# Optimization experiments

Measured on AMD Instinct MI355X. Metric: run time of the kernel, lower is better.

## Reference

```python
import jax, jax.numpy as jnp
import numpy as np

NUM_LAYERS = 6
NUM_HEADS = 8
HIDDEN = 512
GRID_N = 32                      # num_nodes = GRID_N**2 + 1 (encoder pads a global node)
SEQ = GRID_N * GRID_N + 1        # 1025
FFN_HIDDEN = 32 * ((int(2 * HIDDEN / 3) + 31) // 32)  # 352, SwiGLU rounding
BATCH = 8
EPS = 1e-5


def build_grid_mask():
    """4-neighbor grid adjacency + self loops, padded with an all-connected first row/col."""
    n = GRID_N
    idx = np.arange(n * n).reshape(n, n)
    A = np.zeros((n * n, n * n), dtype=bool)
    # horizontal edges
    a, b = idx[:, :-1].ravel(), idx[:, 1:].ravel()
    A[a, b] = True; A[b, a] = True
    # vertical edges
    a, b = idx[:-1, :].ravel(), idx[1:, :].ravel()
    A[a, b] = True; A[b, a] = True
    np.fill_diagonal(A, True)
    M = np.ones((n * n + 1, n * n + 1), dtype=bool)
    M[1:, 1:] = A
    return jnp.asarray(M)


def setup_inputs() -> dict:
    key = jax.random.key(0)
    ks = jax.random.split(key, 9)
    std = 0.02
    D, F, L = HIDDEN, FFN_HIDDEN, NUM_LAYERS
    return {
        "x": jax.random.normal(ks[0], (BATCH, SEQ, D), dtype=jnp.float32),
        "mask": build_grid_mask(),                                  # [SEQ, SEQ] bool
        "wqkv": jax.random.normal(ks[1], (L, 3 * D, D), jnp.float32) * std,
        "wo":   jax.random.normal(ks[2], (L, D, D), jnp.float32) * std,
        "w1":   jax.random.normal(ks[3], (L, F, D), jnp.float32) * std,
        "w2":   jax.random.normal(ks[4], (L, D, F), jnp.float32) * std,
        "w3":   jax.random.normal(ks[5], (L, F, D), jnp.float32) * std,
        "attn_norm_w": jnp.ones((L, D), jnp.float32),
        "ffn_norm_w":  jnp.ones((L, D), jnp.float32),
    }


def rmsnorm(x, w):
    ms = jnp.mean(x * x, axis=-1, keepdims=True)
    return x * jax.lax.rsqrt(ms + EPS) * w


def reference(x, mask, wqkv, wo, w1, w2, w3, attn_norm_w, ffn_norm_w):
    B, S, D = x.shape
    H = NUM_HEADS
    hd = D // H
    scale = 1.0 / jnp.sqrt(jnp.asarray(hd, x.dtype))
    neg = jnp.asarray(-jnp.inf, x.dtype)
    for l in range(NUM_LAYERS):
        # --- attention ---
        h = rmsnorm(x, attn_norm_w[l])
        qkv = h @ wqkv[l].T                                   # [B,S,3D]
        q, k, v = jnp.split(qkv, 3, axis=-1)
        q = q.reshape(B, S, H, hd).transpose(0, 2, 1, 3)      # [B,H,S,hd]
        k = k.reshape(B, S, H, hd).transpose(0, 2, 1, 3)
        v = v.reshape(B, S, H, hd).transpose(0, 2, 1, 3)
        scores = jnp.einsum("bhqd,bhkd->bhqk", q, k) * scale  # [B,H,S,S]
        scores = jnp.where(mask, scores, neg)
        attn = jax.nn.softmax(scores, axis=-1)
        o = jnp.einsum("bhqk,bhkd->bhqd", attn, v)
        o = o.transpose(0, 2, 1, 3).reshape(B, S, D)
        x = x + o @ wo[l].T
        # --- SwiGLU FFN ---
        h = rmsnorm(x, ffn_norm_w[l])
        y = (jax.nn.silu(h @ w1[l].T) * (h @ w3[l].T)) @ w2[l].T
        x = x + y
    return x
```

## Files before the change

kernel.cpp:

```cpp
#include <hip/hip_runtime.h>

typedef unsigned short u16;
typedef short s8v __attribute__((ext_vector_type(8)));
typedef float f4v __attribute__((ext_vector_type(4)));

#define SEQ 1025
#define BATCH 8
#define MROWS (BATCH * SEQ)
#define D 512
#define TD 1536
#define F 352
#define F2I 768
#define FPAD 384
#define NLAYERS 6
#define QKVS ((size_t)BATCH * 8 * SEQ * 64)

__device__ __forceinline__ u16 f2b(float f) {
    unsigned u;
    __builtin_memcpy(&u, &f, 4);
    unsigned r = u + 0x7fffu + ((u >> 16) & 1u);
    return (u16)(r >> 16);
}
__device__ __forceinline__ float b2f(u16 h) {
    unsigned u = ((unsigned)h) << 16;
    float f;
    __builtin_memcpy(&f, &u, 4);
    return f;
}

__global__ __launch_bounds__(256) void convA_k(const float* __restrict__ src, u16* __restrict__ dst, int n4) {
    int i = blockIdx.x * 256 + threadIdx.x;
    if (i >= n4) return;
    float4 v = ((const float4*)src)[i];
    ushort4 r;
    r.x = f2b(v.x); r.y = f2b(v.y); r.z = f2b(v.z); r.w = f2b(v.w);
    ((ushort4*)dst)[i] = r;
}

__global__ __launch_bounds__(256) void convW13i_k(const float* __restrict__ w1, const float* __restrict__ w3, u16* __restrict__ dst) {
    int i = blockIdx.x * 256 + threadIdx.x;
    const int total = NLAYERS * F2I * (D / 4);
    if (i >= total) return;
    int k4 = i & 127;
    int rem = i >> 7;
    int n = rem % F2I, l = rem / F2I;
    int k32 = n >> 5, j = n & 31;
    int f = k32 * 16 + (j & 15);
    ushort4 r;
    if (f < F) {
        const float* src = (j < 16) ? (w1 + ((size_t)(l * F + f) * D))
                                    : (w3 + ((size_t)(l * F + f) * D));
        float4 v = ((const float4*)src)[k4];
        r.x = f2b(v.x); r.y = f2b(v.y); r.z = f2b(v.z); r.w = f2b(v.w);
    } else {
        r.x = 0; r.y = 0; r.z = 0; r.w = 0;
    }
    ((ushort4*)dst)[i] = r;
}

__global__ __launch_bounds__(256) void convW2_k(const float* __restrict__ w2, u16* __restrict__ dst) {
    int i = blockIdx.x * 256 + threadIdx.x;
    const int total = NLAYERS * D * (FPAD / 4);
    if (i >= total) return;
    int k4 = i % (FPAD / 4);
    int rem = i / (FPAD / 4);
    int n = rem % D, l = rem / D;
    ushort4 r;
    if (k4 < F / 4) {
        float4 v = ((const float4*)(w2 + (size_t)(l * D + n) * F))[k4];
        r.x = f2b(v.x); r.y = f2b(v.y); r.z = f2b(v.z); r.w = f2b(v.w);
    } else {
        r.x = 0; r.y = 0; r.z = 0; r.w = 0;
    }
    ((ushort4*)dst)[i] = r;
}

__global__ __launch_bounds__(128) void rmsnorm_k(const float* __restrict__ x, const float* __restrict__ w,
                                                 u16* __restrict__ out) {
    int row = blockIdx.x;
    int tid = threadIdx.x;
    float4 v = ((const float4*)(x + (size_t)row * D))[tid];
    float ss = v.x * v.x + v.y * v.y + v.z * v.z + v.w * v.w;
    #pragma unroll
    for (int off = 32; off; off >>= 1) ss += __shfl_xor(ss, off);
    __shared__ float red[2];
    if ((tid & 63) == 0) red[tid >> 6] = ss;
    __syncthreads();
    float rs = rsqrtf((red[0] + red[1]) * (1.0f / (float)D) + 1e-5f);
    float4 wv = ((const float4*)w)[tid];
    ushort4 pk;
    pk.x = f2b(v.x * rs * wv.x); pk.y = f2b(v.y * rs * wv.y);
    pk.z = f2b(v.z * rs * wv.z); pk.w = f2b(v.w * rs * wv.w);
    ((ushort4*)(out + (size_t)row * D))[tid] = pk;
}

#define STAGE_GEMM(bufofs, kk)                                                          \
    do {                                                                                \
        int k0_ = (kk);                                                                 \
        _Pragma("unroll")                                                               \
        for (int i_ = 0; i_ < 4; ++i_) {                                                \
            int chunk_ = i_ * 256 + tid;                                                \
            int row_ = chunk_ >> 3, kc_ = chunk_ & 7;                                   \
            int gr_ = tm + row_;                                                        \
            gr_ = gr_ < M ? gr_ : M - 1;                                                \
            const u16* srcA_ = A + (size_t)gr_ * K + k0_ + ((kc_ ^ (row_ & 7)) << 3);   \
            __builtin_amdgcn_global_load_lds(                                           \
                (const __attribute__((address_space(1))) void*)srcA_,                   \
                (__attribute__((address_space(3))) void*)(smem + (bufofs) + (size_t)(i_ * 256 + wave * 64) * 8), \
                16, 0, 0);                                                              \
            const u16* srcB_ = B + (size_t)(tn + row_) * K + k0_ + ((kc_ ^ (row_ & 7)) << 3); \
            __builtin_amdgcn_global_load_lds(                                           \
                (const __attribute__((address_space(1))) void*)srcB_,                   \
                (__attribute__((address_space(3))) void*)(smem + 16384 + (bufofs) + (size_t)(i_ * 256 + wave * 64) * 8), \
                16, 0, 0);                                                              \
        }                                                                               \
    } while (0)

template <int MODE>
__global__ __launch_bounds__(256) void gemm_bt_k(const u16* __restrict__ A, const u16* __restrict__ B,
                                                 void* __restrict__ C, int M, int K, int ldc,
                                                 int nx, int nwg) {
    __shared__ u16 smem[32768];
    const int tid = threadIdx.x;
    const int lane = tid & 63;
    const int wave = tid >> 6;
    int hw = blockIdx.x;
    int q8 = nwg >> 3, r8 = nwg & 7;
    int xcd = hw & 7, pos = hw >> 3;
    int work = (xcd < r8 ? xcd * (q8 + 1) : r8 * (q8 + 1) + (xcd - r8) * q8) + pos;
    int ty = work / nx, tx = work - ty * nx;
    const int tm = ty * 128;
    const int tn = tx * 128;
    const int wm = (wave >> 1) * 64;
    const int wn = (wave & 1) * 64;
    f4v acc[4][4] = {};

    const int nk = K >> 6;
    STAGE_GEMM(0, 0);
    __syncthreads();
    for (int k = 0; k < nk; ++k) {
        int cur = (k & 1) * 8192;
        if (k + 1 < nk) STAGE_GEMM(cur ^ 8192, (k + 1) << 6);
        const u16* sa_ = smem + cur;
        const u16* sb_ = smem + 16384 + cur;
        #pragma unroll
        for (int ks = 0; ks < 2; ++ks) {
            int kc = ks * 4 + (lane >> 4);
            s8v af[4], bfr[4];
            #pragma unroll
            for (int mi = 0; mi < 4; ++mi) {
                int row = wm + mi * 16 + (lane & 15);
                af[mi] = *(const s8v*)(sa_ + row * 64 + ((kc ^ (row & 7)) << 3));
            }
            #pragma unroll
            for (int ni = 0; ni < 4; ++ni) {
                int row = wn + ni * 16 + (lane & 15);
                bfr[ni] = *(const s8v*)(sb_ + row * 64 + ((kc ^ (row & 7)) << 3));
            }
            #pragma unroll
            for (int mi = 0; mi < 4; ++mi)
                #pragma unroll
                for (int ni = 0; ni < 4; ++ni)
                    acc[mi][ni] = __builtin_amdgcn_mfma_f32_16x16x32_bf16(af[mi], bfr[ni], acc[mi][ni], 0, 0, 0);
        }
        __syncthreads();
    }

    float* ldsf = (float*)smem;
    #pragma unroll
    for (int mi = 0; mi < 4; ++mi)
        #pragma unroll
        for (int ni = 0; ni < 4; ++ni)
            #pragma unroll
            for (int rr = 0; rr < 4; ++rr) {
                int r = wm + mi * 16 + ((lane >> 4) << 2) + rr;
                int c = wn + ni * 16 + (lane & 15);
                ldsf[r * 128 + c] = acc[mi][ni][rr];
            }
    __syncthreads();

    const int jj = tid & 7;
    #pragma unroll
    for (int pass = 0; pass < 4; ++pass) {
        int r = pass * 32 + (tid >> 3);
        int row = tm + r;
        if (row >= M) continue;
        if (MODE == 1) {
            #pragma unroll
            for (int i = 0; i < 4; ++i) {
                float4 v = *(float4*)&ldsf[r * 128 + i * 32 + jj * 4];
                float* p = (float*)C + (size_t)row * ldc + tn + i * 32 + jj * 4;
                float4 o = *(float4*)p;
                o.x += v.x; o.y += v.y; o.z += v.z; o.w += v.w;
                *(float4*)p = o;
            }
        } else if (MODE == 2) {
            int b = row / SEQ, q = row - b * SEQ;
            #pragma unroll
            for (int i = 0; i < 4; ++i) {
                int col = tn + i * 32 + jj * 4;
                int part = col >> 9, h = (col >> 6) & 7, d = col & 63;
                float4 v = *(float4*)&ldsf[r * 128 + i * 32 + jj * 4];
                ushort4 s;
                s.x = f2b(v.x); s.y = f2b(v.y); s.z = f2b(v.z); s.w = f2b(v.w);
                *(ushort4*)((u16*)C + (size_t)part * QKVS + (((size_t)(b * 8 + h)) * SEQ + q) * 64 + d) = s;
            }
        } else {
            #pragma unroll
            for (int i = 0; i < 4; ++i) {
                float a0 = ldsf[r * 128 + i * 32 + jj * 2];
                float a1 = ldsf[r * 128 + i * 32 + jj * 2 + 1];
                float b0 = ldsf[r * 128 + i * 32 + 16 + jj * 2];
                float b1 = ldsf[r * 128 + i * 32 + 16 + jj * 2 + 1];
                float g0 = a0 / (1.f + __expf(-a0)) * b0;
                float g1 = a1 / (1.f + __expf(-a1)) * b1;
                int f = (tn >> 1) + i * 16 + jj * 2;
                unsigned pk = (unsigned)f2b(g0) | ((unsigned)f2b(g1) << 16);
                *(unsigned*)((u16*)C + (size_t)row * FPAD + f) = pk;
            }
        }
    }
}

__global__ __launch_bounds__(256) void attn_k(const u16* __restrict__ qt, const u16* __restrict__ kt,
                                              const u16* __restrict__ vt, u16* __restrict__ o) {
    const int tid = threadIdx.x;
    if (blockIdx.x >= 64) {
        int sid = blockIdx.x - 64;
        int qtile = sid & 7, bh = sid >> 3;
        int h = bh & 7, b = bh >> 3;
        const size_t slab = (size_t)bh * SEQ * 64;
        const int ql = tid >> 1, half = tid & 1;
        const int q = 1 + qtile * 128 + ql;
        const int q1 = q - 1, r = q1 >> 5, c = q1 & 31;

        const u16* qp = qt + slab + (size_t)q * 64 + half * 32;
        float qf[32];
        #pragma unroll
        for (int cc = 0; cc < 4; ++cc) {
            s8v qv = *(const s8v*)(qp + cc * 8);
            #pragma unroll
            for (int i = 0; i < 8; ++i) qf[cc * 8 + i] = b2f((u16)qv[i]);
        }
        int key[6]; bool valid[6];
        key[0] = 0;      valid[0] = true;
        key[1] = q;      valid[1] = true;
        key[2] = q - 1;  valid[2] = (c > 0);
        key[3] = q + 1;  valid[3] = (c < 31);
        key[4] = q - 32; valid[4] = (r > 0);
        key[5] = q + 32; valid[5] = (r < 31);

        float sc[6];
        #pragma unroll
        for (int j = 0; j < 6; ++j) {
            int kk = valid[j] ? key[j] : 0;
            const u16* kp = kt + slab + (size_t)kk * 64 + half * 32;
            float d = 0.f;
            #pragma unroll
            for (int cc = 0; cc < 4; ++cc) {
                s8v kv = *(const s8v*)(kp + cc * 8);
                #pragma unroll
                for (int i = 0; i < 8; ++i) d += qf[cc * 8 + i] * b2f((u16)kv[i]);
            }
            d += __shfl_xor(d, 1);
            sc[j] = valid[j] ? d * 0.125f : -1e30f;
        }
        float m = sc[0];
        #pragma unroll
        for (int j = 1; j < 6; ++j) m = fmaxf(m, sc[j]);
        float w[6], l = 0.f;
        #pragma unroll
        for (int j = 0; j < 6; ++j) { w[j] = __expf(sc[j] - m); l += w[j]; }
        float inv = 1.f / l;

        float acc[32];
        #pragma unroll
        for (int i = 0; i < 32; ++i) acc[i] = 0.f;
        #pragma unroll
        for (int j = 0; j < 6; ++j) {
            int kk = valid[j] ? key[j] : 0;
            const u16* vp = vt + slab + (size_t)kk * 64 + half * 32;
            #pragma unroll
            for (int cc = 0; cc < 4; ++cc) {
                s8v vv = *(const s8v*)(vp + cc * 8);
                #pragma unroll
                for (int i = 0; i < 8; ++i) acc[cc * 8 + i] += w[j] * b2f((u16)vv[i]);
            }
        }
        u16* orow = o + ((size_t)b * SEQ + q) * D + h * 64 + half * 32;
        #pragma unroll
        for (int cc = 0; cc < 4; ++cc) {
            uint4 pk;
            pk.x = (unsigned)f2b(acc[cc * 8 + 0] * inv) | ((unsigned)f2b(acc[cc * 8 + 1] * inv) << 16);
            pk.y = (unsigned)f2b(acc[cc * 8 + 2] * inv) | ((unsigned)f2b(acc[cc * 8 + 3] * inv) << 16);
            pk.z = (unsigned)f2b(acc[cc * 8 + 4] * inv) | ((unsigned)f2b(acc[cc * 8 + 5] * inv) << 16);
            pk.w = (unsigned)f2b(acc[cc * 8 + 6] * inv) | ((unsigned)f2b(acc[cc * 8 + 7] * inv) << 16);
            *(uint4*)(orow + cc * 8) = pk;
        }
    } else {
        __shared__ float sp[SEQ + 15];
        __shared__ float red[8];
        __shared__ float sacc[4][64];
        int bh = blockIdx.x;
        int h = bh & 7, b = bh >> 3;
        const size_t slab = (size_t)bh * SEQ * 64;
        const int lane = tid & 63, wv = tid >> 6;

        float qf[64];
        #pragma unroll
        for (int cc = 0; cc < 8; ++cc) {
            s8v qv = *(const s8v*)(qt + slab + cc * 8);
            #pragma unroll
            for (int i = 0; i < 8; ++i) qf[cc * 8 + i] = b2f((u16)qv[i]);
        }
        for (int j0 = tid; j0 < SEQ; j0 += 256) {
            const u16* kp = kt + slab + (size_t)j0 * 64;
            float p0 = 0.f, p1 = 0.f, p2 = 0.f, p3 = 0.f;
            #pragma unroll
            for (int cc = 0; cc < 8; ++cc) {
                s8v kv = *(const s8v*)(kp + cc * 8);
                p0 += qf[cc * 8 + 0] * b2f((u16)kv[0]) + qf[cc * 8 + 4] * b2f((u16)kv[4]);
                p1 += qf[cc * 8 + 1] * b2f((u16)kv[1]) + qf[cc * 8 + 5] * b2f((u16)kv[5]);
                p2 += qf[cc * 8 + 2] * b2f((u16)kv[2]) + qf[cc * 8 + 6] * b2f((u16)kv[6]);
                p3 += qf[cc * 8 + 3] * b2f((u16)kv[3]) + qf[cc * 8 + 7] * b2f((u16)kv[7]);
            }
            sp[j0] = ((p0 + p1) + (p2 + p3)) * 0.125f;
        }
        __syncthreads();
        float m = -1e30f;
        for (int j = tid; j < SEQ; j += 256) m = fmaxf(m, sp[j]);
        #pragma unroll
        for (int off = 32; off; off >>= 1) m = fmaxf(m, __shfl_xor(m, off));
        if (lane == 0) red[wv] = m;
        __syncthreads();
        m = fmaxf(fmaxf(red[0], red[1]), fmaxf(red[2], red[3]));
        float lsum = 0.f;
        for (int j = tid; j < SEQ; j += 256) { float e = __expf(sp[j] - m); sp[j] = e; lsum += e; }
        #pragma unroll
        for (int off = 32; off; off >>= 1) lsum += __shfl_xor(lsum, off);
        if (lane == 0) red[4 + wv] = lsum;
        __syncthreads();
        float L = (red[4] + red[5]) + (red[6] + red[7]);
        const int quarter = lane & 3, stripe = lane >> 2;
        float acc[16];
        #pragma unroll
        for (int i = 0; i < 16; ++i) acc[i] = 0.f;
        const int jbase = wv * 256;
        const int njj = (wv == 3) ? 17 : 16;
        for (int jj2 = 0; jj2 < njj; ++jj2) {
            int j = jbase + jj2 * 16 + stripe;
            float wj = (j < SEQ) ? sp[j] : 0.f;
            int je = j < 1024 ? j : 1024;
            const u16* vp = vt + slab + (size_t)je * 64 + quarter * 16;
            s8v v0 = *(const s8v*)(vp);
            s8v v1 = *(const s8v*)(vp + 8);
            #pragma unroll
            for (int i = 0; i < 8; ++i) {
                acc[i]     += wj * b2f((u16)v0[i]);
                acc[8 + i] += wj * b2f((u16)v1[i]);
            }
        }
        #pragma unroll
        for (int off = 4; off <= 32; off <<= 1) {
            #pragma unroll
            for (int i = 0; i < 16; ++i) acc[i] += __shfl_xor(acc[i], off);
        }
        if (lane < 4) {
            #pragma unroll
            for (int i = 0; i < 16; ++i) sacc[wv][lane * 16 + i] = acc[i];
        }
        __syncthreads();
        if (tid < 64) {
            float A = (sacc[0][tid] + sacc[1][tid]) + (sacc[2][tid] + sacc[3][tid]);
            o[((size_t)b * SEQ) * D + h * 64 + tid] = f2b(A / L);
        }
    }
}

extern "C" void kernel_launch(void* const* d_in, const int* in_sizes, int n_in,
                              void* d_out, int out_size, void* d_ws, size_t ws_size,
                              hipStream_t stream) {
    const int M = MROWS;
    const float* x_in = (const float*)d_in[0];
    const float* wqkv = (const float*)d_in[2];
    const float* wo   = (const float*)d_in[3];
    const float* w1   = (const float*)d_in[4];
    const float* w2   = (const float*)d_in[5];
    const float* w3   = (const float*)d_in[6];
    const float* anw  = (const float*)d_in[7];
    const float* fnw  = (const float*)d_in[8];
    float* x = (float*)d_out;

    char* ws = (char*)d_ws;
    auto alloc = [&](size_t n) { char* p = ws; ws += (n + 255) & ~(size_t)255; return p; };
    u16* qkvt  = (u16*)alloc(3 * QKVS * 2);
    u16* hb    = (u16*)alloc((size_t)M * D * 2);
    u16* ob    = (u16*)alloc((size_t)M * D * 2);
    u16* wqkvb = (u16*)alloc((size_t)NLAYERS * TD * D * 2);
    u16* wob   = (u16*)alloc((size_t)NLAYERS * D * D * 2);
    u16* w13b  = (u16*)alloc((size_t)NLAYERS * F2I * D * 2);
    u16* w2b   = (u16*)alloc((size_t)NLAYERS * D * FPAD * 2);
    u16* gp = qkvt;

    hipMemcpyAsync(x, x_in, (size_t)M * D * 4, hipMemcpyDeviceToDevice, stream);

    {
        int n4 = NLAYERS * TD * D / 4;
        convA_k<<<(n4 + 255) / 256, 256, 0, stream>>>(wqkv, wqkvb, n4);
    }
    {
        int n4 = NLAYERS * D * D / 4;
        convA_k<<<(n4 + 255) / 256, 256, 0, stream>>>(wo, wob, n4);
    }
    convW13i_k<<<(NLAYERS * F2I * (D / 4) + 255) / 256, 256, 0, stream>>>(w1, w3, w13b);
    convW2_k<<<(NLAYERS * D * (FPAD / 4) + 255) / 256, 256, 0, stream>>>(w2, w2b);

    const int mt = (M + 127) / 128;
    const int ngQKV = (TD / 128) * mt;
    const int ngD   = (D / 128) * mt;
    const int ngF   = (F2I / 128) * mt;
    for (int l = 0; l < NLAYERS; ++l) {
        rmsnorm_k<<<M, 128, 0, stream>>>(x, anw + (size_t)l * D, hb);
        gemm_bt_k<2><<<ngQKV, 256, 0, stream>>>(hb, wqkvb + (size_t)l * TD * D, qkvt, M, D, TD, TD / 128, ngQKV);
        attn_k<<<64 + 512, 256, 0, stream>>>(qkvt, qkvt + QKVS, qkvt + 2 * QKVS, ob);
        gemm_bt_k<1><<<ngD, 256, 0, stream>>>(ob, wob + (size_t)l * D * D, x, M, D, D, D / 128, ngD);
        rmsnorm_k<<<M, 128, 0, stream>>>(x, fnw + (size_t)l * D, hb);
        gemm_bt_k<3><<<ngF, 256, 0, stream>>>(hb, w13b + (size_t)l * F2I * D, gp, M, D, FPAD, F2I / 128, ngF);
        gemm_bt_k<1><<<ngD, 256, 0, stream>>>(gp, w2b + (size_t)l * D * FPAD, x, M, FPAD, D, D / 128, ngD);
    }
}
```

Baseline: 575.3 us.

## Fuse RMSNorm into GEMM epilogues via folded weights and atomic row sums

```diff
diff --git a/kernel.cpp b/kernel.cpp
--- a/kernel.cpp
+++ b/kernel.cpp
@@ -28,6 +28,21 @@
     return f;
 }
 
+__global__ __launch_bounds__(256) void convQKV_k(const float* __restrict__ wqkv, const float* __restrict__ anw,
+                                                 u16* __restrict__ dst) {
+    int i = blockIdx.x * 256 + threadIdx.x;
+    const int total = NLAYERS * TD * (D / 4);
+    if (i >= total) return;
+    int k4 = i & 127;
+    int rem = i >> 7;
+    int l = rem / TD;
+    float4 v = ((const float4*)wqkv)[i];
+    float4 w = ((const float4*)(anw + (size_t)l * D))[k4];
+    ushort4 r;
+    r.x = f2b(v.x * w.x); r.y = f2b(v.y * w.y); r.z = f2b(v.z * w.z); r.w = f2b(v.w * w.w);
+    ((ushort4*)dst)[i] = r;
+}
+
 __global__ __launch_bounds__(256) void convA_k(const float* __restrict__ src, u16* __restrict__ dst, int n4) {
     int i = blockIdx.x * 256 + threadIdx.x;
     if (i >= n4) return;
@@ -37,7 +52,8 @@
     ((ushort4*)dst)[i] = r;
 }
 
-__global__ __launch_bounds__(256) void convW13i_k(const float* __restrict__ w1, const float* __restrict__ w3, u16* __restrict__ dst) {
+__global__ __launch_bounds__(256) void convW13i_k(const float* __restrict__ w1, const float* __restrict__ w3,
+                                                  const float* __restrict__ fnw, u16* __restrict__ dst) {
     int i = blockIdx.x * 256 + threadIdx.x;
     const int total = NLAYERS * F2I * (D / 4);
     if (i >= total) return;
@@ -51,7 +67,8 @@
         const float* src = (j < 16) ? (w1 + ((size_t)(l * F + f) * D))
                                     : (w3 + ((size_t)(l * F + f) * D));
         float4 v = ((const float4*)src)[k4];
-        r.x = f2b(v.x); r.y = f2b(v.y); r.z = f2b(v.z); r.w = f2b(v.w);
+        float4 w = ((const float4*)(fnw + (size_t)l * D))[k4];
+        r.x = f2b(v.x * w.x); r.y = f2b(v.y * w.y); r.z = f2b(v.z * w.z); r.w = f2b(v.w * w.w);
     } else {
         r.x = 0; r.y = 0; r.z = 0; r.w = 0;
     }
@@ -75,23 +92,29 @@
     ((ushort4*)dst)[i] = r;
 }
 
-__global__ __launch_bounds__(128) void rmsnorm_k(const float* __restrict__ x, const float* __restrict__ w,
-                                                 u16* __restrict__ out) {
+__global__ __launch_bounds__(128) void init_k(const float* __restrict__ xin, float* __restrict__ x,
+                                              u16* __restrict__ xb, float* __restrict__ rs) {
     int row = blockIdx.x;
     int tid = threadIdx.x;
-    float4 v = ((const float4*)(x + (size_t)row * D))[tid];
+    float4 v = ((const float4*)(xin + (size_t)row * D))[tid];
+    ((float4*)(x + (size_t)row * D))[tid] = v;
+    ushort4 pk;
+    pk.x = f2b(v.x); pk.y = f2b(v.y); pk.z = f2b(v.z); pk.w = f2b(v.w);
+    ((ushort4*)(xb + (size_t)row * D))[tid] = pk;
     float ss = v.x * v.x + v.y * v.y + v.z * v.z + v.w * v.w;
     #pragma unroll
     for (int off = 32; off; off >>= 1) ss += __shfl_xor(ss, off);
     __shared__ float red[2];
     if ((tid & 63) == 0) red[tid >> 6] = ss;
     __syncthreads();
-    float rs = rsqrtf((red[0] + red[1]) * (1.0f / (float)D) + 1e-5f);
-    float4 wv = ((const float4*)w)[tid];
-    ushort4 pk;
-    pk.x = f2b(v.x * rs * wv.x); pk.y = f2b(v.y * rs * wv.y);
-    pk.z = f2b(v.z * rs * wv.z); pk.w = f2b(v.w * rs * wv.w);
-    ((ushort4*)(out + (size_t)row * D))[tid] = pk;
+    if (tid == 0) rs[row] = rsqrtf((red[0] + red[1]) * (1.0f / (float)D) + 1e-5f);
+}
+
+__global__ __launch_bounds__(256) void rs_k(float* __restrict__ ssq, float* __restrict__ rs, int M) {
+    int i = blockIdx.x * 256 + threadIdx.x;
+    if (i >= M) return;
+    rs[i] = rsqrtf(ssq[i] * (1.0f / (float)D) + 1e-5f);
+    ssq[i] = 0.f;
 }
 
 #define STAGE_GEMM(bufofs, kk)                                                          \
@@ -118,8 +141,9 @@
 
 template <int MODE>
 __global__ __launch_bounds__(256) void gemm_bt_k(const u16* __restrict__ A, const u16* __restrict__ B,
-                                                 void* __restrict__ C, int M, int K, int ldc,
-                                                 int nx, int nwg) {
+                                                 void* __restrict__ C, const float* __restrict__ rs,
+                                                 float* __restrict__ ssq, u16* __restrict__ xb,
+                                                 int M, int K, int ldc, int nx, int nwg) {
     __shared__ u16 smem[32768];
     const int tid = threadIdx.x;
     const int lane = tid & 63;
@@ -186,15 +210,26 @@
         int row = tm + r;
         if (row >= M) continue;
         if (MODE == 1) {
+            float sumsq = 0.f;
             #pragma unroll
             for (int i = 0; i < 4; ++i) {
                 float4 v = *(float4*)&ldsf[r * 128 + i * 32 + jj * 4];
-                float* p = (float*)C + (size_t)row * ldc + tn + i * 32 + jj * 4;
+                int col = tn + i * 32 + jj * 4;
+                float* p = (float*)C + (size_t)row * ldc + col;
                 float4 o = *(float4*)p;
                 o.x += v.x; o.y += v.y; o.z += v.z; o.w += v.w;
                 *(float4*)p = o;
-            }
+                ushort4 s;
+                s.x = f2b(o.x); s.y = f2b(o.y); s.z = f2b(o.z); s.w = f2b(o.w);
+                *(ushort4*)(xb + (size_t)row * D + col) = s;
+                sumsq += o.x * o.x + o.y * o.y + o.z * o.z + o.w * o.w;
+            }
+            sumsq += __shfl_xor(sumsq, 1);
+            sumsq += __shfl_xor(sumsq, 2);
+            sumsq += __shfl_xor(sumsq, 4);
+            if (jj == 0) atomicAdd(ssq + row, sumsq);
         } else if (MODE == 2) {
+            float s_ = rs[row];
             int b = row / SEQ, q = row - b * SEQ;
             #pragma unroll
             for (int i = 0; i < 4; ++i) {
@@ -202,16 +237,17 @@
                 int part = col >> 9, h = (col >> 6) & 7, d = col & 63;
                 float4 v = *(float4*)&ldsf[r * 128 + i * 32 + jj * 4];
                 ushort4 s;
-                s.x = f2b(v.x); s.y = f2b(v.y); s.z = f2b(v.z); s.w = f2b(v.w);
+                s.x = f2b(v.x * s_); s.y = f2b(v.y * s_); s.z = f2b(v.z * s_); s.w = f2b(v.w * s_);
                 *(ushort4*)((u16*)C + (size_t)part * QKVS + (((size_t)(b * 8 + h)) * SEQ + q) * 64 + d) = s;
             }
         } else {
+            float s_ = rs[row];
             #pragma unroll
             for (int i = 0; i < 4; ++i) {
-                float a0 = ldsf[r * 128 + i * 32 + jj * 2];
-                float a1 = ldsf[r * 128 + i * 32 + jj * 2 + 1];
-                float b0 = ldsf[r * 128 + i * 32 + 16 + jj * 2];
-                float b1 = ldsf[r * 128 + i * 32 + 16 + jj * 2 + 1];
+                float a0 = ldsf[r * 128 + i * 32 + jj * 2] * s_;
+                float a1 = ldsf[r * 128 + i * 32 + jj * 2 + 1] * s_;
+                float b0 = ldsf[r * 128 + i * 32 + 16 + jj * 2] * s_;
+                float b1 = ldsf[r * 128 + i * 32 + 16 + jj * 2 + 1] * s_;
                 float g0 = a0 / (1.f + __expf(-a0)) * b0;
                 float g1 = a1 / (1.f + __expf(-a1)) * b1;
                 int f = (tn >> 1) + i * 16 + jj * 2;
@@ -394,38 +430,38 @@
     char* ws = (char*)d_ws;
     auto alloc = [&](size_t n) { char* p = ws; ws += (n + 255) & ~(size_t)255; return p; };
     u16* qkvt  = (u16*)alloc(3 * QKVS * 2);
-    u16* hb    = (u16*)alloc((size_t)M * D * 2);
+    u16* xb    = (u16*)alloc((size_t)M * D * 2);
     u16* ob    = (u16*)alloc((size_t)M * D * 2);
+    float* rs  = (float*)alloc((size_t)M * 4);
+    float* ssq = (float*)alloc((size_t)M * 4);
     u16* wqkvb = (u16*)alloc((size_t)NLAYERS * TD * D * 2);
     u16* wob   = (u16*)alloc((size_t)NLAYERS * D * D * 2);
     u16* w13b  = (u16*)alloc((size_t)NLAYERS * F2I * D * 2);
     u16* w2b   = (u16*)alloc((size_t)NLAYERS * D * FPAD * 2);
     u16* gp = qkvt;
 
-    hipMemcpyAsync(x, x_in, (size_t)M * D * 4, hipMemcpyDeviceToDevice, stream);
-
-    {
-        int n4 = NLAYERS * TD * D / 4;
-        convA_k<<<(n4 + 255) / 256, 256, 0, stream>>>(wqkv, wqkvb, n4);
-    }
+    hipMemsetAsync(ssq, 0, (size_t)M * 4, stream);
+    convQKV_k<<<(NLAYERS * TD * (D / 4) + 255) / 256, 256, 0, stream>>>(wqkv, anw, wqkvb);
     {
         int n4 = NLAYERS * D * D / 4;
         convA_k<<<(n4 + 255) / 256, 256, 0, stream>>>(wo, wob, n4);
     }
-    convW13i_k<<<(NLAYERS * F2I * (D / 4) + 255) / 256, 256, 0, stream>>>(w1, w3, w13b);
+    convW13i_k<<<(NLAYERS * F2I * (D / 4) + 255) / 256, 256, 0, stream>>>(w1, w3, fnw, w13b);
     convW2_k<<<(NLAYERS * D * (FPAD / 4) + 255) / 256, 256, 0, stream>>>(w2, w2b);
+    init_k<<<M, 128, 0, stream>>>(x_in, x, xb, rs);
 
     const int mt = (M + 127) / 128;
     const int ngQKV = (TD / 128) * mt;
     const int ngD   = (D / 128) * mt;
     const int ngF   = (F2I / 128) * mt;
+    const int ngRS  = (M + 255) / 256;
     for (int l = 0; l < NLAYERS; ++l) {
-        rmsnorm_k<<<M, 128, 0, stream>>>(x, anw + (size_t)l * D, hb);
-        gemm_bt_k<2><<<ngQKV, 256, 0, stream>>>(hb, wqkvb + (size_t)l * TD * D, qkvt, M, D, TD, TD / 128, ngQKV);
+        gemm_bt_k<2><<<ngQKV, 256, 0, stream>>>(xb, wqkvb + (size_t)l * TD * D, qkvt, rs, nullptr, nullptr, M, D, TD, TD / 128, ngQKV);
         attn_k<<<64 + 512, 256, 0, stream>>>(qkvt, qkvt + QKVS, qkvt + 2 * QKVS, ob);
-        gemm_bt_k<1><<<ngD, 256, 0, stream>>>(ob, wob + (size_t)l * D * D, x, M, D, D, D / 128, ngD);
-        rmsnorm_k<<<M, 128, 0, stream>>>(x, fnw + (size_t)l * D, hb);
-        gemm_bt_k<3><<<ngF, 256, 0, stream>>>(hb, w13b + (size_t)l * F2I * D, gp, M, D, FPAD, F2I / 128, ngF);
-        gemm_bt_k<1><<<ngD, 256, 0, stream>>>(gp, w2b + (size_t)l * D * FPAD, x, M, FPAD, D, D / 128, ngD);
-    }
-}
+        gemm_bt_k<1><<<ngD, 256, 0, stream>>>(ob, wob + (size_t)l * D * D, x, nullptr, ssq, xb, M, D, D, D / 128, ngD);
+        rs_k<<<ngRS, 256, 0, stream>>>(ssq, rs, M);
+        gemm_bt_k<3><<<ngF, 256, 0, stream>>>(xb, w13b + (size_t)l * F2I * D, gp, rs, nullptr, nullptr, M, D, FPAD, F2I / 128, ngF);
+        gemm_bt_k<1><<<ngD, 256, 0, stream>>>(gp, w2b + (size_t)l * D * FPAD, x, nullptr, ssq, xb, M, FPAD, D, D / 128, ngD);
+        rs_k<<<ngRS, 256, 0, stream>>>(ssq, rs, M);
+    }
+}
```

Measured after the change: 572.6 us. About the same (-0.5%).
